# Optimization experiments

Hardware: AMD Instinct MI355X
Metric: run time of the kernel (lower is better)

## Reference

```python
import jax, jax.numpy as jnp
import numpy as np

B, D_IN = 16384, 1024
N_DOM, EMB = 4, 16
H1, H2, H3 = 512, 256, 128
FH = 64
EPS = 1e-5


def setup_inputs() -> dict:
    key = jax.random.key(0)
    ks = jax.random.split(key, 32)
    s = 0.02
    def rn(k, shape):
        return jax.random.normal(k, shape, dtype=jnp.float32) * s
    inp = {
        "x": jax.random.normal(ks[0], (B, D_IN), dtype=jnp.float32),
        "domain_ids": jax.random.randint(ks[1], (B,), 0, N_DOM),
        # PartitionedNormalization params
        "pn_w": jnp.ones((N_DOM, D_IN), jnp.float32),
        "pn_b": jnp.zeros((N_DOM, D_IN), jnp.float32),
        # center net: D_IN->512->256->128
        "cW1": rn(ks[2], (D_IN, H1)), "cb1": jnp.zeros((H1,), jnp.float32),
        "cW2": rn(ks[3], (H1, H2)),  "cb2": jnp.zeros((H2,), jnp.float32),
        "cW3": rn(ks[4], (H2, H3)),  "cb3": jnp.zeros((H3,), jnp.float32),
        # domain-specific nets, stacked over domains
        "dW1": rn(ks[5], (N_DOM, D_IN, H1)), "db1": jnp.zeros((N_DOM, H1), jnp.float32),
        "dW2": rn(ks[6], (N_DOM, H1, H2)),  "db2": jnp.zeros((N_DOM, H2), jnp.float32),
        "dW3": rn(ks[7], (N_DOM, H2, H3)),  "db3": jnp.full((N_DOM, H3), 1.0, jnp.float32),  # domain_net_init_bias=1.0
        # final mlp: 128->64->1
        "fW1": rn(ks[8], (H3, FH)), "fb1": jnp.zeros((FH,), jnp.float32),
        "fW2": rn(ks[9], (FH, 1)),  "fb2": jnp.zeros((1,), jnp.float32),
        # domain embedding + auxiliary net: 16->32->1
        "dom_emb": rn(ks[10], (N_DOM, EMB)),
        "aW1": rn(ks[11], (EMB, 32)), "ab1": jnp.zeros((32,), jnp.float32),
        "aW2": rn(ks[12], (32, 1)),   "ab2": jnp.zeros((1,), jnp.float32),
    }
    return inp


def _forward(x, domain_ids, pn_w, pn_b,
             cW1, cb1, cW2, cb2, cW3, cb3,
             dW1, db1, dW2, db2, dW3, db3,
             fW1, fb1, fW2, fb2,
             dom_emb, aW1, ab1, aW2, ab2):
    # Partitioned normalization: per-sample layernorm over features,
    # domain-conditional affine (vectorized gather instead of python loop)
    mean = jnp.mean(x, axis=1, keepdims=True)
    var = jnp.mean(jnp.square(x - mean), axis=1, keepdims=True)  # unbiased=False
    norm = (x - mean) / jnp.sqrt(var + EPS)
    norm = norm * pn_w[domain_ids] + pn_b[domain_ids]  # (B, D_IN)

    # center net
    h = jax.nn.relu(norm @ cW1 + cb1)
    h = jax.nn.relu(h @ cW2 + cb2)
    h_center = h @ cW3 + cb3  # (B, H3)

    # domain-specific nets: compute all domains, then gather per-sample
    hd = jax.nn.relu(jnp.einsum('bi,dio->bdo', norm, dW1) + db1[None])   # (B,D,H1)
    hd = jax.nn.relu(jnp.einsum('bdi,dio->bdo', hd, dW2) + db2[None])    # (B,D,H2)
    hd = jnp.einsum('bdi,dio->bdo', hd, dW3) + db3[None]                 # (B,D,H3)
    h_domain = jnp.take_along_axis(hd, domain_ids[:, None, None], axis=1)[:, 0]  # (B,H3)

    h_fused = h_center * jnp.tanh(h_domain)

    main = jax.nn.relu(h_fused @ fW1 + fb1) @ fW2 + fb2  # (B,1)

    de = dom_emb[domain_ids]                              # (B,EMB)
    aux = jax.nn.relu(de @ aW1 + ab1) @ aW2 + ab2         # (B,1)

    return jax.nn.sigmoid(main + aux)


def reference(x, domain_ids, pn_w, pn_b,
              cW1, cb1, cW2, cb2, cW3, cb3,
              dW1, db1, dW2, db2, dW3, db3,
              fW1, fb1, fW2, fb2,
              dom_emb, aW1, ab1, aW2, ab2):
    return _forward(x, domain_ids, pn_w, pn_b,
                    cW1, cb1, cW2, cb2, cW3, cb3,
                    dW1, db1, dW2, db2, dW3, db3,
                    fW1, fb1, fW2, fb2,
                    dom_emb, aW1, ab1, aW2, ab2)
```

## Files before the change

### kernel.cpp

```cpp
#include <hip/hip_runtime.h>
#include <hip/hip_bf16.h>
#include <stdint.h>

#define NB   16384
#define DIN  1024
#define MPAD 16896

typedef __bf16 bf16;
typedef __bf16 v8bf __attribute__((ext_vector_type(8)));
typedef float  v4f  __attribute__((ext_vector_type(4)));
typedef long   v2l  __attribute__((ext_vector_type(2)));
typedef unsigned char u8;

typedef __attribute__((address_space(1))) void* as1_ptr;
typedef __attribute__((address_space(3))) void* as3_ptr;

__device__ __forceinline__ void gl_lds16(const void* g, void* l) {
  __builtin_amdgcn_global_load_lds((as1_ptr)(g), (as3_ptr)(l), 16, 0, 0);
}

__device__ __forceinline__ unsigned short bfbits(float f) {
  bf16 h = (bf16)f;
  return __builtin_bit_cast(unsigned short, h);
}

__device__ __forceinline__ unsigned short pk8(float a, float b) {
  int u = __builtin_amdgcn_cvt_pk_fp8_f32(a, b, 0, false);
  return (unsigned short)(u & 0xffff);
}

__global__ __launch_bounds__(1024) void k_histscan_aux(
    const int* __restrict__ dom, int* __restrict__ pstart, int* __restrict__ cnt2,
    int* __restrict__ perm, float* __restrict__ aux,
    const float* __restrict__ dom_emb, const float* __restrict__ aW1,
    const float* __restrict__ ab1, const float* __restrict__ aW2,
    const float* __restrict__ ab2) {
  __shared__ int hist[4];
  int tid = threadIdx.x, lane = tid & 63;
  if (tid < 4) hist[tid] = 0;
  if (tid >= 8 && tid < 12) cnt2[tid - 8] = 0;
  for (int j = tid; j < MPAD; j += 1024) perm[j] = -1;
  __syncthreads();
  int c0 = 0, c1 = 0, c2 = 0, c3 = 0;
#pragma unroll
  for (int it = 0; it < 16; it++) {
    int d = dom[it * 1024 + tid];
    c0 += (d == 0); c1 += (d == 1); c2 += (d == 2); c3 += (d == 3);
  }
#pragma unroll
  for (int o = 32; o; o >>= 1) {
    c0 += __shfl_xor(c0, o, 64); c1 += __shfl_xor(c1, o, 64);
    c2 += __shfl_xor(c2, o, 64); c3 += __shfl_xor(c3, o, 64);
  }
  if (lane == 0) {
    atomicAdd(&hist[0], c0); atomicAdd(&hist[1], c1);
    atomicAdd(&hist[2], c2); atomicAdd(&hist[3], c3);
  }
  __syncthreads();
  if (tid == 0) {
    int p = 0;
    for (int d = 0; d < 4; d++) { pstart[d] = p; p += (hist[d] + 127) & ~127; }
    pstart[4] = p;
  }
  if (tid < 4) {
    float a = ab2[0];
    for (int j = 0; j < 32; j++) {
      float s = ab1[j];
      for (int i = 0; i < 16; i++) s += dom_emb[tid * 16 + i] * aW1[i * 32 + j];
      a += fmaxf(s, 0.f) * aW2[j];
    }
    aux[tid] = a;
  }
}

__global__ void k_assign(const int* __restrict__ dom, const int* __restrict__ pstart,
                         int* __restrict__ cnt2, int* __restrict__ perm,
                         int* __restrict__ rowpos) {
  int i = blockIdx.x * 256 + threadIdx.x;
  int lane = threadIdx.x & 63;
  int d = dom[i];
  unsigned long long ltmask = (1ull << lane) - 1ull;
#pragma unroll
  for (int dd = 0; dd < 4; dd++) {
    unsigned long long m = __ballot(d == dd);
    int c = __popcll(m);
    int base = 0;
    if (lane == 0 && c) base = atomicAdd(&cnt2[dd], c);
    base = __shfl(base, 0, 64);
    if (d == dd) {
      int pos = pstart[dd] + base + __popcll(m & ltmask);
      perm[pos] = i;
      rowpos[i] = pos;
    }
  }
}

__global__ __launch_bounds__(256) void k_ln(const float* __restrict__ x,
                                            const int* __restrict__ dom,
                                            const int* __restrict__ rowpos,
                                            const float* __restrict__ pn_w,
                                            const float* __restrict__ pn_b,
                                            u8* __restrict__ norm) {
  int wv = threadIdx.x >> 6, lane = threadIdx.x & 63;
  int r = blockIdx.x * 4 + wv;
  const float* xr = x + (size_t)r * DIN;
  float4 v[4];
#pragma unroll
  for (int g = 0; g < 4; g++) v[g] = *(const float4*)(xr + g * 256 + lane * 4);
  float s = 0.f;
#pragma unroll
  for (int g = 0; g < 4; g++) s += v[g].x + v[g].y + v[g].z + v[g].w;
#pragma unroll
  for (int o = 32; o; o >>= 1) s += __shfl_xor(s, o, 64);
  float mean = s * (1.f / 1024.f);
  float q = 0.f;
#pragma unroll
  for (int g = 0; g < 4; g++) {
    float a = v[g].x - mean, b = v[g].y - mean, c = v[g].z - mean, e = v[g].w - mean;
    q += a * a + b * b + c * c + e * e;
  }
#pragma unroll
  for (int o = 32; o; o >>= 1) q += __shfl_xor(q, o, 64);
  float rstd = rsqrtf(q * (1.f / 1024.f) + 1e-5f);
  int d = dom[r];
  int pos = rowpos[r];
  const float* pw = pn_w + (size_t)d * DIN;
  const float* pb = pn_b + (size_t)d * DIN;
  u8* orow = norm + (size_t)pos * DIN;
#pragma unroll
  for (int g = 0; g < 4; g++) {
    float4 w4 = *(const float4*)(pw + g * 256 + lane * 4);
    float4 b4 = *(const float4*)(pb + g * 256 + lane * 4);
    float f0 = (v[g].x - mean) * rstd * w4.x + b4.x;
    float f1 = (v[g].y - mean) * rstd * w4.y + b4.y;
    float f2 = (v[g].z - mean) * rstd * w4.z + b4.z;
    float f3 = (v[g].w - mean) * rstd * w4.w + b4.w;
    int u = __builtin_amdgcn_cvt_pk_fp8_f32(f0, f1, 0, false);
    u = __builtin_amdgcn_cvt_pk_fp8_f32(f2, f3, u, true);
    *(unsigned int*)(orow + g * 256 + lane * 4) = (unsigned int)u;
  }
}

__global__ __launch_bounds__(256) void k_wt_all(
    const float* __restrict__ cW1, const float* __restrict__ cW2,
    const float* __restrict__ cW3, const float* __restrict__ dW1,
    const float* __restrict__ dW2, const float* __restrict__ dW3,
    const float* __restrict__ fW1,
    u8* __restrict__ cW1t, u8* __restrict__ cW2t, u8* __restrict__ cW3t,
    u8* __restrict__ dW1t, u8* __restrict__ dW2t, u8* __restrict__ dW3t,
    bf16* __restrict__ fW1t) {
  __shared__ float t[64 * 65];
  int bid = blockIdx.x;
  const float* src; u8* dst; int K, N, tile; bool isf = false;
  if (bid < 640) {
    K = 1024; N = 512; int m = bid >> 7; tile = bid & 127;
    src = m == 0 ? cW1 : dW1 + (size_t)(m - 1) * 524288;
    dst = m == 0 ? cW1t : dW1t + (size_t)(m - 1) * 524288;
  } else if (bid < 800) {
    K = 512; N = 256; int m = (bid - 640) >> 5; tile = (bid - 640) & 31;
    src = m == 0 ? cW2 : dW2 + (size_t)(m - 1) * 131072;
    dst = m == 0 ? cW2t : dW2t + (size_t)(m - 1) * 131072;
  } else if (bid < 840) {
    K = 256; N = 128; int m = (bid - 800) >> 3; tile = (bid - 800) & 7;
    src = m == 0 ? cW3 : dW3 + (size_t)(m - 1) * 32768;
    dst = m == 0 ? cW3t : dW3t + (size_t)(m - 1) * 32768;
  } else {
    K = 128; N = 64; tile = bid - 840; src = fW1; dst = nullptr; isf = true;
  }
  int ntn = N >> 6;
  int k0 = (tile / ntn) << 6, n0 = (tile % ntn) << 6;
  int tid = threadIdx.x;
  int r = tid >> 2, c4 = (tid & 3) << 4;
#pragma unroll
  for (int j4 = 0; j4 < 4; j4++) {
    float4 v = *(const float4*)(src + (size_t)(k0 + r) * N + n0 + c4 + j4 * 4);
    t[r * 65 + c4 + j4 * 4 + 0] = v.x;
    t[r * 65 + c4 + j4 * 4 + 1] = v.y;
    t[r * 65 + c4 + j4 * 4 + 2] = v.z;
    t[r * 65 + c4 + j4 * 4 + 3] = v.w;
  }
  __syncthreads();
  int n = tid >> 2, kc = (tid & 3) << 4;
  if (!isf) {
#pragma unroll
    for (int j4 = 0; j4 < 4; j4++) {
      float v0 = t[(kc + j4 * 4 + 0) * 65 + n] * 16.f;
      float v1 = t[(kc + j4 * 4 + 1) * 65 + n] * 16.f;
      float v2 = t[(kc + j4 * 4 + 2) * 65 + n] * 16.f;
      float v3 = t[(kc + j4 * 4 + 3) * 65 + n] * 16.f;
      int u = __builtin_amdgcn_cvt_pk_fp8_f32(v0, v1, 0, false);
      u = __builtin_amdgcn_cvt_pk_fp8_f32(v2, v3, u, true);
      *(unsigned int*)(dst + (size_t)(n0 + n) * K + k0 + kc + j4 * 4) = (unsigned int)u;
    }
  } else {
#pragma unroll
    for (int j4 = 0; j4 < 4; j4++) {
      ushort4 o;
      o.x = bfbits(t[(kc + j4 * 4 + 0) * 65 + n]);
      o.y = bfbits(t[(kc + j4 * 4 + 1) * 65 + n]);
      o.z = bfbits(t[(kc + j4 * 4 + 2) * 65 + n]);
      o.w = bfbits(t[(kc + j4 * 4 + 3) * 65 + n]);
      *(ushort4*)(fW1t + (size_t)(n0 + n) * K + k0 + kc + j4 * 4) = o;
    }
  }
}

__global__ __launch_bounds__(256) void k_gemm(const u8* __restrict__ A, int lda,
                                              int aoffc, int aoffd,
                                              const u8* __restrict__ cWt,
                                              const u8* __restrict__ dWt,
                                              const float* __restrict__ cb,
                                              const float* __restrict__ db,
                                              u8* __restrict__ C, int Nh, int Kd,
                                              int relu, const int* __restrict__ pstart,
                                              int lognct) {
  __shared__ __align__(16) u8 Al[64 * 128];
  __shared__ __align__(16) u8 Bl[128 * 128];
  const int tid = threadIdx.x;
  const int wv = tid >> 6, lane = tid & 63;
  const int nct = 1 << lognct;
  int l = blockIdx.x;
  int t = l >> 3;
  int ct = t & (nct - 1);
  int rt = ((t >> lognct) << 3) | (l & 7);
  const int row0 = rt * 64;
  const int d = (row0 >= pstart[1]) + (row0 >= pstart[2]) + (row0 >= pstart[3]);
  const int n0 = ct * 128;
  const bool isd = (n0 >= Nh);
  const u8* Wt = isd ? dWt + ((size_t)d * Nh + (n0 - Nh)) * Kd : cWt + (size_t)n0 * Kd;
  const float* bias = isd ? db + d * Nh + (n0 - Nh) : cb + n0;
  const int aoff = isd ? aoffd : aoffc;
  const u8* Ab = A + (size_t)row0 * lda + aoff;

  v4f acc[2][4];
#pragma unroll
  for (int i = 0; i < 2; i++)
#pragma unroll
    for (int j = 0; j < 4; j++) acc[i][j] = v4f{0.f, 0.f, 0.f, 0.f};

  const int wm = (wv >> 1) * 32, wn = (wv & 1) * 64;
  const int mrow = lane & 15, quad = lane >> 4;
  const int lrow = lane >> 3;
  const int lchk = lane & 7;
  const int ldc = 2 * Nh;

  for (int kt = 0; kt < Kd; kt += 128) {
#pragma unroll
    for (int p = 0; p < 2; p++) {
      int rbase = wv * 16 + p * 8;
      int r = rbase + lrow;
      int jg = lchk ^ (r & 7);
      gl_lds16(Ab + (size_t)r * lda + kt + jg * 16, &Al[rbase * 128]);
    }
#pragma unroll
    for (int p = 0; p < 4; p++) {
      int rbase = wv * 32 + p * 8;
      int r = rbase + lrow;
      int jg = lchk ^ (r & 7);
      gl_lds16(Wt + (size_t)r * Kd + kt + jg * 16, &Bl[rbase * 128]);
    }
    __syncthreads();
#pragma unroll
    for (int sp = 0; sp < 2; sp++) {
      v2l af[2], bfr[4];
#pragma unroll
      for (int mi = 0; mi < 2; mi++) {
        int m = wm + mi * 16 + mrow;
        int c = (sp * 4 + quad) ^ (m & 7);
        af[mi] = *(const v2l*)&Al[m * 128 + c * 16];
      }
#pragma unroll
      for (int ni = 0; ni < 4; ni++) {
        int n = wn + ni * 16 + mrow;
        int c = (sp * 4 + quad) ^ (n & 7);
        bfr[ni] = *(const v2l*)&Bl[n * 128 + c * 16];
      }
#pragma unroll
      for (int mi = 0; mi < 2; mi++)
#pragma unroll
        for (int ni = 0; ni < 4; ni++)
          acc[mi][ni] =
              __builtin_amdgcn_mfma_f32_16x16x32_fp8_fp8(af[mi].x, bfr[ni].x, acc[mi][ni], 0, 0, 0);
#pragma unroll
      for (int mi = 0; mi < 2; mi++)
#pragma unroll
        for (int ni = 0; ni < 4; ni++)
          acc[mi][ni] =
              __builtin_amdgcn_mfma_f32_16x16x32_fp8_fp8(af[mi].y, bfr[ni].y, acc[mi][ni], 0, 0, 0);
    }
    __syncthreads();
  }

  float bv[4];
#pragma unroll
  for (int ni = 0; ni < 4; ni++) bv[ni] = bias[wn + ni * 16 + mrow];
#pragma unroll
  for (int mi = 0; mi < 2; mi++) {
    int growb = row0 + wm + mi * 16 + quad * 4;
#pragma unroll
    for (int ni = 0; ni < 4; ni++) {
      int gcol = n0 + wn + ni * 16 + mrow;
#pragma unroll
      for (int r2 = 0; r2 < 4; r2++) {
        float v = acc[mi][ni][r2] * 0.0625f + bv[ni];
        if (relu) v = fmaxf(v, 0.f);
        float g = __shfl_xor(v, 1, 64);
        if (!(mrow & 1))
          *(unsigned short*)(C + (size_t)(growb + r2) * ldc + gcol) = pk8(v, g);
      }
    }
  }
}

__global__ __launch_bounds__(256) void k_gemm3(const u8* __restrict__ A,
                                               const u8* __restrict__ cW3t,
                                               const u8* __restrict__ dW3t,
                                               const float* __restrict__ cb3,
                                               const float* __restrict__ db3,
                                               const bf16* __restrict__ fW1t,
                                               const float* __restrict__ fb1,
                                               const float* __restrict__ fW2,
                                               const float* __restrict__ fb2,
                                               const int* __restrict__ perm,
                                               const int* __restrict__ pstart,
                                               const float* __restrict__ aux,
                                               float* __restrict__ out) {
  __shared__ __align__(16) u8 Al[64 * 128];
  __shared__ __align__(16) u8 Bl[128 * 128];
  __shared__ __align__(16) bf16 fusedL[64 * 128];
  __shared__ __align__(16) bf16 fwB[64 * 128];
  const int tid = threadIdx.x, wv = tid >> 6, lane = tid & 63;
  const int row0 = blockIdx.x * 64;
  const int d = (row0 >= pstart[1]) + (row0 >= pstart[2]) + (row0 >= pstart[3]);
  const u8* Ab = A + (size_t)row0 * 512;
  const int mrow = lane & 15, quad = lane >> 4;
  const int lrow = lane >> 3, lchk = lane & 7;
  const int wm = (wv >> 1) * 32, wn = (wv & 1) * 64;

  {
    int c = lane & 15, rsub = lane >> 4;
#pragma unroll
    for (int p = 0; p < 4; p++) {
      int rbase = wv * 16 + p * 4;
      int row = rbase + rsub;
      int g = (c & 8) | ((c ^ row) & 7);
      gl_lds16(fW1t + row * 128 + g * 8, &fwB[rbase * 128]);
    }
  }

  v4f accC[2][4], accD[2][4];
#pragma unroll
  for (int i = 0; i < 2; i++)
#pragma unroll
    for (int j = 0; j < 4; j++) { accC[i][j] = v4f{0.f,0.f,0.f,0.f}; accD[i][j] = v4f{0.f,0.f,0.f,0.f}; }

#pragma unroll
  for (int ph = 0; ph < 2; ph++) {
    const u8* Wt = ph ? dW3t + (size_t)d * 32768 : cW3t;
    const int aoff = ph * 256;
    for (int kt = 0; kt < 256; kt += 128) {
#pragma unroll
      for (int p = 0; p < 2; p++) {
        int rbase = wv * 16 + p * 8;
        int r = rbase + lrow;
        int jg = lchk ^ (r & 7);
        gl_lds16(Ab + (size_t)r * 512 + aoff + kt + jg * 16, &Al[rbase * 128]);
      }
#pragma unroll
      for (int p = 0; p < 4; p++) {
        int rbase = wv * 32 + p * 8;
        int r = rbase + lrow;
        int jg = lchk ^ (r & 7);
        gl_lds16(Wt + (size_t)r * 256 + kt + jg * 16, &Bl[rbase * 128]);
      }
      __syncthreads();
#pragma unroll
      for (int sp = 0; sp < 2; sp++) {
        v2l af[2], bfr[4];
#pragma unroll
        for (int mi = 0; mi < 2; mi++) {
          int m = wm + mi * 16 + mrow;
          int c = (sp * 4 + quad) ^ (m & 7);
          af[mi] = *(const v2l*)&Al[m * 128 + c * 16];
        }
#pragma unroll
        for (int ni = 0; ni < 4; ni++) {
          int n = wn + ni * 16 + mrow;
          int c = (sp * 4 + quad) ^ (n & 7);
          bfr[ni] = *(const v2l*)&Bl[n * 128 + c * 16];
        }
        if (ph == 0) {
#pragma unroll
          for (int mi = 0; mi < 2; mi++)
#pragma unroll
            for (int ni = 0; ni < 4; ni++) {
              accC[mi][ni] = __builtin_amdgcn_mfma_f32_16x16x32_fp8_fp8(af[mi].x, bfr[ni].x, accC[mi][ni], 0, 0, 0);
              accC[mi][ni] = __builtin_amdgcn_mfma_f32_16x16x32_fp8_fp8(af[mi].y, bfr[ni].y, accC[mi][ni], 0, 0, 0);
            }
        } else {
#pragma unroll
          for (int mi = 0; mi < 2; mi++)
#pragma unroll
            for (int ni = 0; ni < 4; ni++) {
              accD[mi][ni] = __builtin_amdgcn_mfma_f32_16x16x32_fp8_fp8(af[mi].x, bfr[ni].x, accD[mi][ni], 0, 0, 0);
              accD[mi][ni] = __builtin_amdgcn_mfma_f32_16x16x32_fp8_fp8(af[mi].y, bfr[ni].y, accD[mi][ni], 0, 0, 0);
            }
        }
      }
      __syncthreads();
    }
  }

#pragma unroll
  for (int mi = 0; mi < 2; mi++) {
    int rowb = wm + mi * 16 + quad * 4;
#pragma unroll
    for (int ni = 0; ni < 4; ni++) {
      int col = wn + ni * 16 + mrow;
      float cbv = cb3[col];
      float dbv = db3[d * 128 + col];
      int jc = col >> 3, coff = col & 7;
#pragma unroll
      for (int r2 = 0; r2 < 4; r2++) {
        int rr = rowb + r2;
        float f = (accC[mi][ni][r2] * 0.0625f + cbv) * tanhf(accD[mi][ni][r2] * 0.0625f + dbv);
        int cs = (jc & 8) | ((jc ^ rr) & 7);
        fusedL[rr * 128 + cs * 8 + coff] = (bf16)f;
      }
    }
  }
  __syncthreads();

  float fb1v[4], fW2v[4];
#pragma unroll
  for (int nt = 0; nt < 4; nt++) {
    int col = nt * 16 + mrow;
    fb1v[nt] = fb1[col];
    fW2v[nt] = fW2[col];
  }
  v4f hacc[4];
#pragma unroll
  for (int nt = 0; nt < 4; nt++) hacc[nt] = v4f{0.f, 0.f, 0.f, 0.f};
  const int m = wv * 16 + mrow;
#pragma unroll
  for (int s = 0; s < 4; s++) {
    int j = s * 4 + quad;
    int ca = (j & 8) | ((j ^ m) & 7);
    v8bf af = *(const v8bf*)&fusedL[m * 128 + ca * 8];
#pragma unroll
    for (int nt = 0; nt < 4; nt++) {
      int n = nt * 16 + mrow;
      int cbk = (j & 8) | ((j ^ n) & 7);
      v8bf bfr = *(const v8bf*)&fwB[n * 128 + cbk * 8];
      hacc[nt] = __builtin_amdgcn_mfma_f32_16x16x32_bf16(af, bfr, hacc[nt], 0, 0, 0);
    }
  }
  float ys[4];
#pragma unroll
  for (int r2 = 0; r2 < 4; r2++) {
    float s = 0.f;
#pragma unroll
    for (int nt = 0; nt < 4; nt++) s += fmaxf(hacc[nt][r2] + fb1v[nt], 0.f) * fW2v[nt];
    ys[r2] = s;
  }
#pragma unroll
  for (int o = 1; o < 16; o <<= 1)
#pragma unroll
    for (int r2 = 0; r2 < 4; r2++) ys[r2] += __shfl_xor(ys[r2], o, 64);
  if (mrow == 0) {
    const float addc = fb2[0] + aux[d];
#pragma unroll
    for (int r2 = 0; r2 < 4; r2++) {
      int prow = row0 + wv * 16 + quad * 4 + r2;
      int orig = perm[prow];
      if (orig >= 0) out[orig] = 1.f / (1.f + expf(-(ys[r2] + addc)));
    }
  }
}

extern "C" void kernel_launch(void* const* d_in, const int* in_sizes, int n_in,
                              void* d_out, int out_size, void* d_ws, size_t ws_size,
                              hipStream_t stream) {
  (void)in_sizes; (void)n_in; (void)out_size; (void)ws_size;
  const float* x      = (const float*)d_in[0];
  const int*   dom    = (const int*)d_in[1];
  const float* pn_w   = (const float*)d_in[2];
  const float* pn_b   = (const float*)d_in[3];
  const float* cW1    = (const float*)d_in[4];
  const float* cb1    = (const float*)d_in[5];
  const float* cW2    = (const float*)d_in[6];
  const float* cb2    = (const float*)d_in[7];
  const float* cW3    = (const float*)d_in[8];
  const float* cb3    = (const float*)d_in[9];
  const float* dW1    = (const float*)d_in[10];
  const float* db1    = (const float*)d_in[11];
  const float* dW2    = (const float*)d_in[12];
  const float* db2    = (const float*)d_in[13];
  const float* dW3    = (const float*)d_in[14];
  const float* db3    = (const float*)d_in[15];
  const float* fW1    = (const float*)d_in[16];
  const float* fb1    = (const float*)d_in[17];
  const float* fW2    = (const float*)d_in[18];
  const float* fb2    = (const float*)d_in[19];
  const float* demb   = (const float*)d_in[20];
  const float* aW1    = (const float*)d_in[21];
  const float* ab1    = (const float*)d_in[22];
  const float* aW2    = (const float*)d_in[23];
  const float* ab2    = (const float*)d_in[24];
  float* out = (float*)d_out;

  char* w = (char*)d_ws;
  int*   cnt2   = (int*)(w + 0);
  int*   pstart = (int*)(w + 32);
  float* aux    = (float*)(w + 64);
  int*   perm   = (int*)(w + 256);
  int*   rowpos = (int*)(w + 67840);
  u8*    bufA   = (u8*)(w + 133376);
  u8*    bufB   = (u8*)(w + 17434880);
  u8*    cW1t   = (u8*)(w + 34736384);
  u8*    cW2t   = (u8*)(w + 35260672);
  u8*    cW3t   = (u8*)(w + 35391744);
  u8*    dW1t   = (u8*)(w + 35424512);
  u8*    dW2t   = (u8*)(w + 37521664);
  u8*    dW3t   = (u8*)(w + 38045952);
  bf16*  fW1t   = (bf16*)(w + 38177024);

  k_histscan_aux<<<1, 1024, 0, stream>>>(dom, pstart, cnt2, perm, aux,
                                         demb, aW1, ab1, aW2, ab2);
  k_assign<<<64, 256, 0, stream>>>(dom, pstart, cnt2, perm, rowpos);
  k_ln<<<4096, 256, 0, stream>>>(x, dom, rowpos, pn_w, pn_b, bufA);
  k_wt_all<<<842, 256, 0, stream>>>(cW1, cW2, cW3, dW1, dW2, dW3, fW1,
                                    cW1t, cW2t, cW3t, dW1t, dW2t, dW3t, fW1t);

  k_gemm<<<2112, 256, 0, stream>>>(bufA, 1024, 0, 0, cW1t, dW1t, cb1, db1,
                                   bufB, 512, 1024, 1, pstart, 3);
  k_gemm<<<1056, 256, 0, stream>>>(bufB, 1024, 0, 512, cW2t, dW2t, cb2, db2,
                                   bufA, 256, 512, 1, pstart, 2);
  k_gemm3<<<264, 256, 0, stream>>>(bufA, cW3t, dW3t, cb3, db3, fW1t,
                                   fb1, fW2, fb2, perm, pstart, aux, out);
}
```

Measured before the change: 235.1 us.

## Fuse domain sort, aux, weight prep and layernorm into two kernels

Replaces the single-block histogram kernel, the atomic assign kernel, the layernorm kernel and the weight-transpose kernel with two launches. The first does the weight transposes and also writes per-16-row domain counts, the perm padding fill and the aux values. The second has each block prefix-sum those counts to place its 16 rows, writes perm and pstart, then runs layernorm straight into sorted positions. This removes two launches, the serial one-block histogram and the global atomics, and makes the row order deterministic. In exchange every sortln block redundantly scans all 4096 partial counts.

```diff
diff --git a/kernel.cpp b/kernel.cpp
--- a/kernel.cpp
+++ b/kernel.cpp
@@ -29,128 +29,48 @@
   return (unsigned short)(u & 0xffff);
 }
 
-__global__ __launch_bounds__(1024) void k_histscan_aux(
-    const int* __restrict__ dom, int* __restrict__ pstart, int* __restrict__ cnt2,
-    int* __restrict__ perm, float* __restrict__ aux,
-    const float* __restrict__ dom_emb, const float* __restrict__ aW1,
-    const float* __restrict__ ab1, const float* __restrict__ aW2,
-    const float* __restrict__ ab2) {
-  __shared__ int hist[4];
-  int tid = threadIdx.x, lane = tid & 63;
-  if (tid < 4) hist[tid] = 0;
-  if (tid >= 8 && tid < 12) cnt2[tid - 8] = 0;
-  for (int j = tid; j < MPAD; j += 1024) perm[j] = -1;
-  __syncthreads();
-  int c0 = 0, c1 = 0, c2 = 0, c3 = 0;
-#pragma unroll
-  for (int it = 0; it < 16; it++) {
-    int d = dom[it * 1024 + tid];
-    c0 += (d == 0); c1 += (d == 1); c2 += (d == 2); c3 += (d == 3);
-  }
-#pragma unroll
-  for (int o = 32; o; o >>= 1) {
-    c0 += __shfl_xor(c0, o, 64); c1 += __shfl_xor(c1, o, 64);
-    c2 += __shfl_xor(c2, o, 64); c3 += __shfl_xor(c3, o, 64);
-  }
-  if (lane == 0) {
-    atomicAdd(&hist[0], c0); atomicAdd(&hist[1], c1);
-    atomicAdd(&hist[2], c2); atomicAdd(&hist[3], c3);
-  }
-  __syncthreads();
-  if (tid == 0) {
-    int p = 0;
-    for (int d = 0; d < 4; d++) { pstart[d] = p; p += (hist[d] + 127) & ~127; }
-    pstart[4] = p;
-  }
-  if (tid < 4) {
-    float a = ab2[0];
-    for (int j = 0; j < 32; j++) {
-      float s = ab1[j];
-      for (int i = 0; i < 16; i++) s += dom_emb[tid * 16 + i] * aW1[i * 32 + j];
-      a += fmaxf(s, 0.f) * aW2[j];
-    }
-    aux[tid] = a;
-  }
-}
-
-__global__ void k_assign(const int* __restrict__ dom, const int* __restrict__ pstart,
-                         int* __restrict__ cnt2, int* __restrict__ perm,
-                         int* __restrict__ rowpos) {
-  int i = blockIdx.x * 256 + threadIdx.x;
-  int lane = threadIdx.x & 63;
-  int d = dom[i];
-  unsigned long long ltmask = (1ull << lane) - 1ull;
-#pragma unroll
-  for (int dd = 0; dd < 4; dd++) {
-    unsigned long long m = __ballot(d == dd);
-    int c = __popcll(m);
-    int base = 0;
-    if (lane == 0 && c) base = atomicAdd(&cnt2[dd], c);
-    base = __shfl(base, 0, 64);
-    if (d == dd) {
-      int pos = pstart[dd] + base + __popcll(m & ltmask);
-      perm[pos] = i;
-      rowpos[i] = pos;
-    }
-  }
-}
-
-__global__ __launch_bounds__(256) void k_ln(const float* __restrict__ x,
-                                            const int* __restrict__ dom,
-                                            const int* __restrict__ rowpos,
-                                            const float* __restrict__ pn_w,
-                                            const float* __restrict__ pn_b,
-                                            u8* __restrict__ norm) {
-  int wv = threadIdx.x >> 6, lane = threadIdx.x & 63;
-  int r = blockIdx.x * 4 + wv;
-  const float* xr = x + (size_t)r * DIN;
-  float4 v[4];
-#pragma unroll
-  for (int g = 0; g < 4; g++) v[g] = *(const float4*)(xr + g * 256 + lane * 4);
-  float s = 0.f;
-#pragma unroll
-  for (int g = 0; g < 4; g++) s += v[g].x + v[g].y + v[g].z + v[g].w;
-#pragma unroll
-  for (int o = 32; o; o >>= 1) s += __shfl_xor(s, o, 64);
-  float mean = s * (1.f / 1024.f);
-  float q = 0.f;
-#pragma unroll
-  for (int g = 0; g < 4; g++) {
-    float a = v[g].x - mean, b = v[g].y - mean, c = v[g].z - mean, e = v[g].w - mean;
-    q += a * a + b * b + c * c + e * e;
-  }
-#pragma unroll
-  for (int o = 32; o; o >>= 1) q += __shfl_xor(q, o, 64);
-  float rstd = rsqrtf(q * (1.f / 1024.f) + 1e-5f);
-  int d = dom[r];
-  int pos = rowpos[r];
-  const float* pw = pn_w + (size_t)d * DIN;
-  const float* pb = pn_b + (size_t)d * DIN;
-  u8* orow = norm + (size_t)pos * DIN;
-#pragma unroll
-  for (int g = 0; g < 4; g++) {
-    float4 w4 = *(const float4*)(pw + g * 256 + lane * 4);
-    float4 b4 = *(const float4*)(pb + g * 256 + lane * 4);
-    float f0 = (v[g].x - mean) * rstd * w4.x + b4.x;
-    float f1 = (v[g].y - mean) * rstd * w4.y + b4.y;
-    float f2 = (v[g].z - mean) * rstd * w4.z + b4.z;
-    float f3 = (v[g].w - mean) * rstd * w4.w + b4.w;
-    int u = __builtin_amdgcn_cvt_pk_fp8_f32(f0, f1, 0, false);
-    u = __builtin_amdgcn_cvt_pk_fp8_f32(f2, f3, u, true);
-    *(unsigned int*)(orow + g * 256 + lane * 4) = (unsigned int)u;
-  }
-}
-
-__global__ __launch_bounds__(256) void k_wt_all(
+__global__ __launch_bounds__(256) void k_prep(
     const float* __restrict__ cW1, const float* __restrict__ cW2,
     const float* __restrict__ cW3, const float* __restrict__ dW1,
     const float* __restrict__ dW2, const float* __restrict__ dW3,
     const float* __restrict__ fW1,
     u8* __restrict__ cW1t, u8* __restrict__ cW2t, u8* __restrict__ cW3t,
     u8* __restrict__ dW1t, u8* __restrict__ dW2t, u8* __restrict__ dW3t,
-    bf16* __restrict__ fW1t) {
+    bf16* __restrict__ fW1t,
+    const int* __restrict__ dom, int* __restrict__ partials, int* __restrict__ perm,
+    const float* __restrict__ dom_emb, const float* __restrict__ aW1,
+    const float* __restrict__ ab1, const float* __restrict__ aW2,
+    const float* __restrict__ ab2, float* __restrict__ aux) {
   __shared__ float t[64 * 65];
   int bid = blockIdx.x;
+  int tid = threadIdx.x;
+  if (bid >= 842) {
+    int b2 = bid - 842;
+    int wv = tid >> 6, lane = tid & 63;
+    int row = b2 * 256 + tid;
+    int d = dom[row];
+    int gbase = b2 * 16 + wv * 4;
+#pragma unroll
+    for (int dd = 0; dd < 4; dd++) {
+      unsigned long long m = __ballot(d == dd);
+      int q = lane >> 4;
+      int cnt = __popcll((m >> (16 * q)) & 0xFFFFull);
+      if ((lane & 15) == 0) partials[(gbase + q) * 4 + dd] = cnt;
+    }
+    for (int j = b2 * 264 + tid; j < b2 * 264 + 264; j += 256)
+      if (j < MPAD) perm[j] = -1;
+    if (b2 == 0 && tid >= 64 && tid < 68) {
+      int dd = tid - 64;
+      float a = ab2[0];
+      for (int j = 0; j < 32; j++) {
+        float s = ab1[j];
+        for (int i = 0; i < 16; i++) s += dom_emb[dd * 16 + i] * aW1[i * 32 + j];
+        a += fmaxf(s, 0.f) * aW2[j];
+      }
+      aux[dd] = a;
+    }
+    return;
+  }
   const float* src; u8* dst; int K, N, tile; bool isf = false;
   if (bid < 640) {
     K = 1024; N = 512; int m = bid >> 7; tile = bid & 127;
@@ -169,7 +89,6 @@
   }
   int ntn = N >> 6;
   int k0 = (tile / ntn) << 6, n0 = (tile % ntn) << 6;
-  int tid = threadIdx.x;
   int r = tid >> 2, c4 = (tid & 3) << 4;
 #pragma unroll
   for (int j4 = 0; j4 < 4; j4++) {
@@ -201,6 +120,93 @@
       o.z = bfbits(t[(kc + j4 * 4 + 2) * 65 + n]);
       o.w = bfbits(t[(kc + j4 * 4 + 3) * 65 + n]);
       *(ushort4*)(fW1t + (size_t)(n0 + n) * K + k0 + kc + j4 * 4) = o;
+    }
+  }
+}
+
+__global__ __launch_bounds__(256) void k_sortln(
+    const float* __restrict__ x, const int* __restrict__ dom,
+    const int* __restrict__ partials,
+    const float* __restrict__ pn_w, const float* __restrict__ pn_b,
+    int* __restrict__ pstart_g, int* __restrict__ perm, u8* __restrict__ norm) {
+  __shared__ int totL[4], preL[4];
+  __shared__ int posL[16];
+  const int tid = threadIdx.x, wv = tid >> 6, lane = tid & 63;
+  const int B = blockIdx.x;
+  int tot = 0, pre = 0;
+  for (int g = lane; g < 1024; g += 64) {
+    int v = partials[g * 4 + wv];
+    tot += v;
+    if (g < B) pre += v;
+  }
+#pragma unroll
+  for (int o = 32; o; o >>= 1) {
+    tot += __shfl_xor(tot, o, 64);
+    pre += __shfl_xor(pre, o, 64);
+  }
+  if (lane == 0) { totL[wv] = tot; preL[wv] = pre; }
+  __syncthreads();
+  const int p1 = (totL[0] + 127) & ~127;
+  const int p2 = p1 + ((totL[1] + 127) & ~127);
+  const int p3 = p2 + ((totL[2] + 127) & ~127);
+  if (B == 0 && tid < 5) {
+    int ps0 = (tid == 0) ? 0 : (tid == 1 ? p1 : (tid == 2 ? p2 : (tid == 3 ? p3
+              : p3 + ((totL[3] + 127) & ~127))));
+    pstart_g[tid] = ps0;
+  }
+  if (wv == 0 && lane < 16) {
+    int row = B * 16 + lane;
+    int d = dom[row];
+    unsigned long long ltm = (1ull << lane) - 1ull;
+    int pstA[4] = {0, p1, p2, p3};
+    int pos = 0;
+#pragma unroll
+    for (int dd = 0; dd < 4; dd++) {
+      unsigned long long m = __ballot(d == dd);
+      if (d == dd) pos = pstA[dd] + preL[dd] + (int)__popcll(m & ltm);
+    }
+    posL[lane] = pos;
+    perm[pos] = row;
+  }
+  __syncthreads();
+  for (int i = 0; i < 4; i++) {
+    int ridx = wv * 4 + i;
+    int r = B * 16 + ridx;
+    const float* xr = x + (size_t)r * DIN;
+    float4 v[4];
+#pragma unroll
+    for (int g = 0; g < 4; g++) v[g] = *(const float4*)(xr + g * 256 + lane * 4);
+    float s = 0.f;
+#pragma unroll
+    for (int g = 0; g < 4; g++) s += v[g].x + v[g].y + v[g].z + v[g].w;
+#pragma unroll
+    for (int o = 32; o; o >>= 1) s += __shfl_xor(s, o, 64);
+    float mean = s * (1.f / 1024.f);
+    float q = 0.f;
+#pragma unroll
+    for (int g = 0; g < 4; g++) {
+      float a = v[g].x - mean, b = v[g].y - mean, c = v[g].z - mean, e = v[g].w - mean;
+      q += a * a + b * b + c * c + e * e;
+    }
+#pragma unroll
+    for (int o = 32; o; o >>= 1) q += __shfl_xor(q, o, 64);
+    float rstd = rsqrtf(q * (1.f / 1024.f) + 1e-5f);
+    int d = dom[r];
+    int pos = posL[ridx];
+    const float* pw = pn_w + (size_t)d * DIN;
+    const float* pb = pn_b + (size_t)d * DIN;
+    u8* orow = norm + (size_t)pos * DIN;
+#pragma unroll
+    for (int g = 0; g < 4; g++) {
+      float4 w4 = *(const float4*)(pw + g * 256 + lane * 4);
+      float4 b4 = *(const float4*)(pb + g * 256 + lane * 4);
+      float f0 = (v[g].x - mean) * rstd * w4.x + b4.x;
+      float f1 = (v[g].y - mean) * rstd * w4.y + b4.y;
+      float f2 = (v[g].z - mean) * rstd * w4.z + b4.z;
+      float f3 = (v[g].w - mean) * rstd * w4.w + b4.w;
+      int u = __builtin_amdgcn_cvt_pk_fp8_f32(f0, f1, 0, false);
+      u = __builtin_amdgcn_cvt_pk_fp8_f32(f2, f3, u, true);
+      *(unsigned int*)(orow + g * 256 + lane * 4) = (unsigned int)u;
     }
   }
 }
@@ -510,27 +516,26 @@
   float* out = (float*)d_out;
 
   char* w = (char*)d_ws;
-  int*   cnt2   = (int*)(w + 0);
-  int*   pstart = (int*)(w + 32);
-  float* aux    = (float*)(w + 64);
-  int*   perm   = (int*)(w + 256);
-  int*   rowpos = (int*)(w + 67840);
-  u8*    bufA   = (u8*)(w + 133376);
-  u8*    bufB   = (u8*)(w + 17434880);
-  u8*    cW1t   = (u8*)(w + 34736384);
-  u8*    cW2t   = (u8*)(w + 35260672);
-  u8*    cW3t   = (u8*)(w + 35391744);
-  u8*    dW1t   = (u8*)(w + 35424512);
-  u8*    dW2t   = (u8*)(w + 37521664);
-  u8*    dW3t   = (u8*)(w + 38045952);
-  bf16*  fW1t   = (bf16*)(w + 38177024);
-
-  k_histscan_aux<<<1, 1024, 0, stream>>>(dom, pstart, cnt2, perm, aux,
-                                         demb, aW1, ab1, aW2, ab2);
-  k_assign<<<64, 256, 0, stream>>>(dom, pstart, cnt2, perm, rowpos);
-  k_ln<<<4096, 256, 0, stream>>>(x, dom, rowpos, pn_w, pn_b, bufA);
-  k_wt_all<<<842, 256, 0, stream>>>(cW1, cW2, cW3, dW1, dW2, dW3, fW1,
-                                    cW1t, cW2t, cW3t, dW1t, dW2t, dW3t, fW1t);
+  int*   pstart  = (int*)(w + 32);
+  float* aux     = (float*)(w + 64);
+  int*   perm    = (int*)(w + 256);
+  int*   partials= (int*)(w + 67840);
+  u8*    bufA    = (u8*)(w + 133376);
+  u8*    bufB    = (u8*)(w + 17434880);
+  u8*    cW1t    = (u8*)(w + 34736384);
+  u8*    cW2t    = (u8*)(w + 35260672);
+  u8*    cW3t    = (u8*)(w + 35391744);
+  u8*    dW1t    = (u8*)(w + 35424512);
+  u8*    dW2t    = (u8*)(w + 37521664);
+  u8*    dW3t    = (u8*)(w + 38045952);
+  bf16*  fW1t    = (bf16*)(w + 38177024);
+
+  k_prep<<<906, 256, 0, stream>>>(cW1, cW2, cW3, dW1, dW2, dW3, fW1,
+                                  cW1t, cW2t, cW3t, dW1t, dW2t, dW3t, fW1t,
+                                  dom, partials, perm,
+                                  demb, aW1, ab1, aW2, ab2, aux);
+  k_sortln<<<1024, 256, 0, stream>>>(x, dom, partials, pn_w, pn_b,
+                                     pstart, perm, bufA);
 
   k_gemm<<<2112, 256, 0, stream>>>(bufA, 1024, 0, 0, cW1t, dW1t, cb1, db1,
                                    bufB, 512, 1024, 1, pstart, 3);
```

Result: faster. 224.6 us, median of 2 (-4.5%).
